# Kernel optimization log

Hardware: AMD Instinct MI355X
Metric: run time of the kernel (lower is better)

Reference implementation:

```python
import jax, jax.numpy as jnp
import numpy as np
from jax import lax

B, L, D_IN, H, D_OUT = 128, 1024, 64, 512, 64


def setup_inputs() -> dict:
    key = jax.random.key(0)
    ks = jax.random.split(key, 11)
    s_in = 1.0 / np.sqrt(D_IN)
    s_h = 1.0 / np.sqrt(H)
    return {
        "u": jax.random.normal(ks[0], (B, L, D_IN), jnp.float32),
        "W_in": jax.random.uniform(ks[1], (H, D_IN), jnp.float32, -s_in, s_in),
        "W_ih0": jax.random.uniform(ks[2], (H, H), jnp.float32, -s_h, s_h),
        "W_hh0": jax.random.uniform(ks[3], (H, H), jnp.float32, -s_h, s_h),
        "b_ih0": jax.random.uniform(ks[4], (H,), jnp.float32, -s_h, s_h),
        "b_hh0": jax.random.uniform(ks[5], (H,), jnp.float32, -s_h, s_h),
        "W_ih1": jax.random.uniform(ks[6], (H, H), jnp.float32, -s_h, s_h),
        "W_hh1": jax.random.uniform(ks[7], (H, H), jnp.float32, -s_h, s_h),
        "b_ih1": jax.random.uniform(ks[8], (H,), jnp.float32, -s_h, s_h),
        "b_hh1": jax.random.uniform(ks[9], (H,), jnp.float32, -s_h, s_h),
        "W_out": jax.random.uniform(ks[10], (D_OUT, H), jnp.float32, -s_h, s_h),
    }


def _rnn_layer(x, W_ih, W_hh, b):
    # x: [B, L, H]. Precompute input contribution as one big GEMM.
    xw = jnp.einsum("blh,gh->blg", x, W_ih) + b  # [B, L, H]
    xw_t = jnp.swapaxes(xw, 0, 1)  # [L, B, H] for scan over time

    def step(h, xt):
        h_new = jnp.tanh(xt + h @ W_hh.T)
        return h_new, h_new

    h0 = jnp.zeros((x.shape[0], W_hh.shape[0]), x.dtype)
    _, ys = lax.scan(step, h0, xw_t)
    return jnp.swapaxes(ys, 0, 1)  # [B, L, H]


def reference(u, W_in, W_ih0, W_hh0, b_ih0, b_hh0, W_ih1, W_hh1, b_ih1, b_hh1, W_out):
    x = jnp.einsum("bld,hd->blh", u, W_in)  # proj_in (no bias)
    x = _rnn_layer(x, W_ih0, W_hh0, b_ih0 + b_hh0)
    x = _rnn_layer(x, W_ih1, W_hh1, b_ih1 + b_hh1)
    y = jnp.einsum("blh,oh->blo", x, W_out)  # proj_out (no bias)
    return y
```

## Files before the change

### kernel.cpp

```cpp
#include <hip/hip_runtime.h>
#include <hip/hip_fp16.h>

#define B_   128
#define L_   1024
#define DIN  64
#define H_   512
#define DOUT 64

typedef _Float16 half8 __attribute__((ext_vector_type(8)));
typedef float    f32x4 __attribute__((ext_vector_type(4)));

#define FSTR 16
#define SPIN_CAP (1<<16)
#define POLL_CAP (1<<15)
#define POISON   0x7C00u

#define MFMA16(a,b,c) __builtin_amdgcn_mfma_f32_16x16x32_f16((a),(b),(c),0,0,0)
#define PINH8(x) asm volatile("" : "+v"(x))
#define AGENT_ST(p, v) __hip_atomic_store((p), (v), __ATOMIC_RELAXED, __HIP_MEMORY_SCOPE_AGENT)
#define AGENT_LD(p)    __hip_atomic_load((p), __ATOMIC_RELAXED, __HIP_MEMORY_SCOPE_AGENT)

__global__ void k_init(int* flags, unsigned int* hx0u, unsigned int* hx1u) {
    int i = blockIdx.x * blockDim.x + threadIdx.x;
    const int NR = 8 * 8 * 8192 / 2;
    if (i < NR) { hx0u[i] = 0x7C007C00u; hx1u[i] = 0x7C007C00u; }
    if (i < 104) flags[i * FSTR] = -1;
}

__global__ void k_prep_w(const float* __restrict__ whh0, const float* __restrict__ wih1,
                         const float* __restrict__ whh1, const float* __restrict__ wout,
                         const float* __restrict__ bih0, const float* __restrict__ bhh0,
                         const float* __restrict__ bih1, const float* __restrict__ bhh1,
                         _Float16* __restrict__ o0, _Float16* __restrict__ o1,
                         _Float16* __restrict__ o2, _Float16* __restrict__ o3,
                         float* __restrict__ b0s, float* __restrict__ b1s) {
    const int NW = H_ * H_;
    const int total = 3 * NW + DOUT * H_ + 2 * H_;
    int i  = blockIdx.x * blockDim.x + threadIdx.x;
    int st = gridDim.x * blockDim.x;
    for (; i < total; i += st) {
        if      (i < NW)            o0[i]          = (_Float16)whh0[i];
        else if (i < 2 * NW)        o1[i - NW]     = (_Float16)wih1[i - NW];
        else if (i < 3 * NW)        o2[i - 2 * NW] = (_Float16)whh1[i - 2 * NW];
        else if (i < 3 * NW + DOUT * H_) o3[i - 3 * NW] = (_Float16)wout[i - 3 * NW];
        else if (i < 3 * NW + DOUT * H_ + H_) {
            int j = i - (3 * NW + DOUT * H_);
            b0s[j] = bih0[j] + bhh0[j];
        } else {
            int j = i - (3 * NW + DOUT * H_ + H_);
            b1s[j] = bih1[j] + bhh1[j];
        }
    }
}

__global__ void k_wcomb(const float* __restrict__ wih0, const float* __restrict__ win,
                        _Float16* __restrict__ o) {
    int g = blockIdx.x;
    int d = threadIdx.x;
    float acc = 0.f;
    for (int h = 0; h < H_; ++h)
        acc += wih0[g * H_ + h] * win[h * DIN + d];
    o[g * DIN + d] = (_Float16)acc;
}

__device__ __forceinline__ int spin_geq(const int* fp, int tgt, int cached) {
    if (cached >= tgt) return cached;
    int v = AGENT_LD(fp);
    int it = 0;
    while (v < tgt && ++it < SPIN_CAP) v = AGENT_LD(fp);
    return v;
}

__device__ __forceinline__ float tanh_fast(float v) {
    float e = __expf(2.f * v);
    return 1.f - 2.f / (e + 1.f);
}

__device__ __forceinline__ void st16_sc(void* p, half8 v) {
    asm volatile("global_store_dwordx4 %0, %1, off sc0 sc1" :: "v"(p), "v"(v) : "memory");
}

__device__ __forceinline__ void ld4_sc(const _Float16* p0, const _Float16* p1,
                                       const _Float16* p2, const _Float16* p3,
                                       half8& a, half8& b, half8& c, half8& d) {
    asm volatile(
        "global_load_dwordx4 %0, %4, off sc0 sc1\n\t"
        "global_load_dwordx4 %1, %5, off sc0 sc1\n\t"
        "global_load_dwordx4 %2, %6, off sc0 sc1\n\t"
        "global_load_dwordx4 %3, %7, off sc0 sc1\n\t"
        "s_waitcnt vmcnt(0)"
        : "=&v"(a), "=&v"(b), "=&v"(c), "=&v"(d)
        : "v"(p0), "v"(p1), "v"(p2), "v"(p3) : "memory");
}
__device__ __forceinline__ void ld8_sc(const _Float16* p0, const _Float16* p1,
                                       const _Float16* p2, const _Float16* p3,
                                       const _Float16* p4, const _Float16* p5,
                                       const _Float16* p6, const _Float16* p7,
                                       half8& a, half8& b, half8& c, half8& d,
                                       half8& e, half8& f, half8& g, half8& h) {
    asm volatile(
        "global_load_dwordx4 %0, %8, off sc0 sc1\n\t"
        "global_load_dwordx4 %1, %9, off sc0 sc1\n\t"
        "global_load_dwordx4 %2, %10, off sc0 sc1\n\t"
        "global_load_dwordx4 %3, %11, off sc0 sc1\n\t"
        "global_load_dwordx4 %4, %12, off sc0 sc1\n\t"
        "global_load_dwordx4 %5, %13, off sc0 sc1\n\t"
        "global_load_dwordx4 %6, %14, off sc0 sc1\n\t"
        "global_load_dwordx4 %7, %15, off sc0 sc1\n\t"
        "s_waitcnt vmcnt(0)"
        : "=&v"(a), "=&v"(b), "=&v"(c), "=&v"(d),
          "=&v"(e), "=&v"(f), "=&v"(g), "=&v"(h)
        : "v"(p0), "v"(p1), "v"(p2), "v"(p3),
          "v"(p4), "v"(p5), "v"(p6), "v"(p7) : "memory");
}

__device__ __forceinline__ int chunk_ok(half8 h) {
    union { half8 v; unsigned short s[8]; } u; u.v = h;
    return u.s[0] != POISON;
}

__global__ __launch_bounds__(256, 1)
void k_pipeline(const float* __restrict__ u,
                const _Float16* __restrict__ wcomb,
                const _Float16* __restrict__ whh0w,
                const float* __restrict__ b0s,
                const _Float16* __restrict__ wih1w,
                const _Float16* __restrict__ whh1w,
                const float* __restrict__ b1s,
                const _Float16* __restrict__ woutw,
                float* __restrict__ out,
                _Float16* __restrict__ hx0,
                _Float16* __restrict__ hx1,
                int* __restrict__ flags) {
    const int bid = blockIdx.x;
    const int g = bid & 7, role = bid >> 3;
    const int tid = threadIdx.x;
    const int l = tid & 63, w = tid >> 6;
    const int l15 = l & 15, lg = l >> 4, kofs = lg * 8;
    const int b0 = g * 16;
    _Float16* hx0g = hx0 + (size_t)g * 65536;
    _Float16* hx1g = hx1 + (size_t)g * 65536;
    int* myctr = flags + bid * FSTR;

    __shared__ _Float16 pb0[16][520];
    __shared__ _Float16 pb1[16][520];
    __shared__ _Float16 hlt[16][136];

    union { unsigned short s[8]; half8 h; } pv;
#pragma unroll
    for (int i = 0; i < 8; ++i) pv.s[i] = POISON;
    const half8 poisonv = pv.h;

    const int rof0 = tid * 8;
    const int rof1 = rof0 + 2048;
    const int rof2 = rof0 + 4096;
    const int rof3 = rof0 + 6144;
    const int prw = tid >> 6;
    const int pcol = (tid & 63) * 8;

    if (role < 4) {
        const int s = role;
        const int col0 = s * 128 + w * 32;
        half8 whf[2][16], wcf[2][2];
#pragma unroll
        for (int nt = 0; nt < 2; ++nt) {
            const int n = col0 + nt * 16 + l15;
#pragma unroll
            for (int kt = 0; kt < 16; ++kt) {
                whf[nt][kt] = *(const half8*)(whh0w + (size_t)n * H_ + kt * 32 + kofs);
                PINH8(whf[nt][kt]);
            }
#pragma unroll
            for (int kt = 0; kt < 2; ++kt) {
                wcf[nt][kt] = *(const half8*)(wcomb + (size_t)n * DIN + kt * 32 + kofs);
                PINH8(wcf[nt][kt]);
            }
        }
        const float bv0 = b0s[col0 + l15], bv1 = b0s[col0 + 16 + l15];
        const int* gate = (tid < 12) ? flags + (g + 8 * tid) * FSTR : nullptr;
        int gcache = -1;
        const int oofs = (tid >> 4) * 512 + s * 128 + (tid & 15) * 8;

        for (int t = 0; t < L_; ++t) {
            if (t >= 4 && (t & 3) == 0 && gate) gcache = spin_geq(gate, t - 3, gcache);
            __syncthreads();
            st16_sc(hx0g + (size_t)((t + 2) & 7) * 8192 + oofs, poisonv);
            const float* up = u + ((size_t)(b0 + l15) * L_ + t) * DIN + kofs;
            f32x4 u0 = *(const f32x4*)(up);
            f32x4 u1 = *(const f32x4*)(up + 4);
            f32x4 u2 = *(const f32x4*)(up + 32);
            f32x4 u3 = *(const f32x4*)(up + 36);
            half8 ua0, ua1;
#pragma unroll
            for (int j = 0; j < 4; ++j) {
                ua0[j] = (_Float16)u0[j]; ua0[4 + j] = (_Float16)u1[j];
                ua1[j] = (_Float16)u2[j]; ua1[4 + j] = (_Float16)u3[j];
            }
            f32x4 acc0 = (f32x4){bv0, bv0, bv0, bv0};
            f32x4 acc1 = (f32x4){bv1, bv1, bv1, bv1};
            acc0 = MFMA16(ua0, wcf[0][0], acc0); acc0 = MFMA16(ua1, wcf[0][1], acc0);
            acc1 = MFMA16(ua0, wcf[1][0], acc1); acc1 = MFMA16(ua1, wcf[1][1], acc1);
            if (t > 0) {
                const _Float16* sb = hx0g + (size_t)((t - 1) & 7) * 8192;
                half8 c0, c1, c2, c3; int it = 0;
                for (;;) {
                    ld4_sc(sb + rof0, sb + rof1, sb + rof2, sb + rof3, c0, c1, c2, c3);
                    if ((chunk_ok(c0) & chunk_ok(c1) & chunk_ok(c2) & chunk_ok(c3))
                        || ++it > POLL_CAP) break;
                }
                *(half8*)&pb0[prw][pcol]      = c0;
                *(half8*)&pb0[prw + 4][pcol]  = c1;
                *(half8*)&pb0[prw + 8][pcol]  = c2;
                *(half8*)&pb0[prw + 12][pcol] = c3;
            }
            __syncthreads();
            if (tid == 0) AGENT_ST(myctr, t);
            if (t > 0) {
#pragma unroll
                for (int kt = 0; kt < 16; ++kt) {
                    half8 a = *(const half8*)&pb0[l15][kt * 32 + kofs];
                    acc0 = MFMA16(a, whf[0][kt], acc0);
                    acc1 = MFMA16(a, whf[1][kt], acc1);
                }
            }
            _Float16 th0[4], th1[4];
#pragma unroll
            for (int r = 0; r < 4; ++r) {
                th0[r] = (_Float16)tanh_fast(acc0[r]);
                th1[r] = (_Float16)tanh_fast(acc1[r]);
            }
#pragma unroll
            for (int r = 0; r < 4; ++r) {
                hlt[lg * 4 + r][w * 32 + l15]      = th0[r];
                hlt[lg * 4 + r][w * 32 + 16 + l15] = th1[r];
            }
            __syncthreads();
            half8 ch = *(const half8*)&hlt[tid >> 4][(tid & 15) * 8];
            asm volatile("s_waitcnt vmcnt(0)" ::: "memory");
            st16_sc(hx0g + (size_t)(t & 7) * 8192 + oofs, ch);
        }
    } else if (role < 12) {
        const int s = role - 4;
        const int n = s * 64 + w * 16 + l15;
        half8 wif[16], whf1[16];
#pragma unroll
        for (int kt = 0; kt < 16; ++kt) {
            wif[kt] = *(const half8*)(wih1w + (size_t)n * H_ + kt * 32 + kofs);
            PINH8(wif[kt]);
            whf1[kt] = *(const half8*)(whh1w + (size_t)n * H_ + kt * 32 + kofs);
            PINH8(whf1[kt]);
        }
        const float bv = b1s[n];
        const int* gate = (tid < 9) ? flags + (g + 8 * (4 + tid)) * FSTR : nullptr;
        int gcache = -1;
        const int oofs = (tid >> 3) * 512 + s * 64 + (tid & 7) * 8;

        for (int t = 0; t < L_; ++t) {
            if (t >= 4 && (t & 3) == 0 && gate) gcache = spin_geq(gate, t - 3, gcache);
            __syncthreads();
            if (tid < 128)
                st16_sc(hx1g + (size_t)((t + 2) & 7) * 8192 + oofs, poisonv);
            const _Float16* s0 = hx0g + (size_t)(t & 7) * 8192;
            if (t > 0) {
                const _Float16* s1 = hx1g + (size_t)((t - 1) & 7) * 8192;
                half8 d0, d1, d2, d3, e0, e1, e2, e3; int it = 0;
                for (;;) {
                    ld8_sc(s1 + rof0, s1 + rof1, s1 + rof2, s1 + rof3,
                           s0 + rof0, s0 + rof1, s0 + rof2, s0 + rof3,
                           d0, d1, d2, d3, e0, e1, e2, e3);
                    if ((chunk_ok(d0) & chunk_ok(d1) & chunk_ok(d2) & chunk_ok(d3)
                       & chunk_ok(e0) & chunk_ok(e1) & chunk_ok(e2) & chunk_ok(e3))
                        || ++it > POLL_CAP) break;
                }
                *(half8*)&pb1[prw][pcol]      = d0;
                *(half8*)&pb1[prw + 4][pcol]  = d1;
                *(half8*)&pb1[prw + 8][pcol]  = d2;
                *(half8*)&pb1[prw + 12][pcol] = d3;
                *(half8*)&pb0[prw][pcol]      = e0;
                *(half8*)&pb0[prw + 4][pcol]  = e1;
                *(half8*)&pb0[prw + 8][pcol]  = e2;
                *(half8*)&pb0[prw + 12][pcol] = e3;
            } else {
                half8 e0, e1, e2, e3; int it = 0;
                for (;;) {
                    ld4_sc(s0 + rof0, s0 + rof1, s0 + rof2, s0 + rof3, e0, e1, e2, e3);
                    if ((chunk_ok(e0) & chunk_ok(e1) & chunk_ok(e2) & chunk_ok(e3))
                        || ++it > POLL_CAP) break;
                }
                *(half8*)&pb0[prw][pcol]      = e0;
                *(half8*)&pb0[prw + 4][pcol]  = e1;
                *(half8*)&pb0[prw + 8][pcol]  = e2;
                *(half8*)&pb0[prw + 12][pcol] = e3;
            }
            __syncthreads();
            if (tid == 0) AGENT_ST(myctr, t);
            f32x4 acch = (f32x4){0.f, 0.f, 0.f, 0.f};
            f32x4 accx = (f32x4){bv, bv, bv, bv};
            if (t > 0) {
#pragma unroll
                for (int kt = 0; kt < 16; ++kt) {
                    half8 a1 = *(const half8*)&pb1[l15][kt * 32 + kofs];
                    acch = MFMA16(a1, whf1[kt], acch);
                    half8 a0 = *(const half8*)&pb0[l15][kt * 32 + kofs];
                    accx = MFMA16(a0, wif[kt], accx);
                }
            } else {
#pragma unroll
                for (int kt = 0; kt < 16; ++kt) {
                    half8 a0 = *(const half8*)&pb0[l15][kt * 32 + kofs];
                    accx = MFMA16(a0, wif[kt], accx);
                }
            }
            _Float16 th[4];
#pragma unroll
            for (int r = 0; r < 4; ++r) th[r] = (_Float16)tanh_fast(accx[r] + acch[r]);
#pragma unroll
            for (int r = 0; r < 4; ++r)
                hlt[lg * 4 + r][w * 16 + l15] = th[r];
            __syncthreads();
            if (tid < 128) {
                half8 ch = *(const half8*)&hlt[tid >> 3][(tid & 7) * 8];
                asm volatile("s_waitcnt vmcnt(0)" ::: "memory");
                st16_sc(hx1g + (size_t)(t & 7) * 8192 + oofs, ch);
            }
        }
    } else {
        const int n = w * 16 + l15;
        half8 wof[16];
#pragma unroll
        for (int kt = 0; kt < 16; ++kt) {
            wof[kt] = *(const half8*)(woutw + (size_t)n * H_ + kt * 32 + kofs);
            PINH8(wof[kt]);
        }
        for (int t = 0; t < L_; ++t) {
            __syncthreads();
            const _Float16* sb = hx1g + (size_t)(t & 7) * 8192;
            half8 c0, c1, c2, c3; int it = 0;
            for (;;) {
                ld4_sc(sb + rof0, sb + rof1, sb + rof2, sb + rof3, c0, c1, c2, c3);
                if ((chunk_ok(c0) & chunk_ok(c1) & chunk_ok(c2) & chunk_ok(c3))
                    || ++it > POLL_CAP) break;
            }
            *(half8*)&pb1[prw][pcol]      = c0;
            *(half8*)&pb1[prw + 4][pcol]  = c1;
            *(half8*)&pb1[prw + 8][pcol]  = c2;
            *(half8*)&pb1[prw + 12][pcol] = c3;
            __syncthreads();
            if (tid == 0) AGENT_ST(myctr, t);
            f32x4 acc = (f32x4){0.f, 0.f, 0.f, 0.f};
#pragma unroll
            for (int kt = 0; kt < 16; ++kt) {
                half8 a = *(const half8*)&pb1[l15][kt * 32 + kofs];
                acc = MFMA16(a, wof[kt], acc);
            }
#pragma unroll
            for (int r = 0; r < 4; ++r)
                out[((size_t)(b0 + lg * 4 + r) * L_ + t) * DOUT + n] = acc[r];
        }
    }
}

extern "C" void kernel_launch(void* const* d_in, const int* in_sizes, int n_in,
                              void* d_out, int out_size, void* d_ws, size_t ws_size,
                              hipStream_t stream) {
    const float* u    = (const float*)d_in[0];
    const float* Win  = (const float*)d_in[1];
    const float* Wih0 = (const float*)d_in[2];
    const float* Whh0 = (const float*)d_in[3];
    const float* bih0 = (const float*)d_in[4];
    const float* bhh0 = (const float*)d_in[5];
    const float* Wih1 = (const float*)d_in[6];
    const float* Whh1 = (const float*)d_in[7];
    const float* bih1 = (const float*)d_in[8];
    const float* bhh1 = (const float*)d_in[9];
    const float* Wout = (const float*)d_in[10];
    (void)in_sizes; (void)n_in; (void)out_size; (void)ws_size;

    char* ws = (char*)d_ws;
    size_t off = 0;
    auto alloc = [&](size_t bytes) {
        char* p = ws + off;
        off += (bytes + 255) & ~(size_t)255;
        return p;
    };
    _Float16* wcomb = (_Float16*)alloc((size_t)H_ * DIN * 2);
    _Float16* whh0h = (_Float16*)alloc((size_t)H_ * H_ * 2);
    _Float16* wih1h = (_Float16*)alloc((size_t)H_ * H_ * 2);
    _Float16* whh1h = (_Float16*)alloc((size_t)H_ * H_ * 2);
    _Float16* wouth = (_Float16*)alloc((size_t)DOUT * H_ * 2);
    float*    b0s   = (float*)alloc(H_ * 4);
    float*    b1s   = (float*)alloc(H_ * 4);
    _Float16* hx0   = (_Float16*)alloc((size_t)8 * 8 * 8192 * 2);
    _Float16* hx1   = (_Float16*)alloc((size_t)8 * 8 * 8192 * 2);
    int*      flags = (int*)alloc(104 * FSTR * 4);

    k_init<<<1024, 256, 0, stream>>>(flags, (unsigned int*)hx0, (unsigned int*)hx1);
    k_prep_w<<<1024, 256, 0, stream>>>(Whh0, Wih1, Whh1, Wout, bih0, bhh0, bih1, bhh1,
                                       whh0h, wih1h, whh1h, wouth, b0s, b1s);
    k_wcomb<<<512, 64, 0, stream>>>(Wih0, Win, wcomb);

    k_pipeline<<<104, 256, 0, stream>>>(u, wcomb, whh0h, b0s, wih1h, whh1h, b1s, wouth,
                                        (float*)d_out, hx0, hx1, flags);
}
```

Measured before the change: 2.380 ms.

## Merge per-step barriers, prefetch next u row, and pin weights inside loop

Removes the leading __syncthreads of each time step in all roles by moving the flow-control spin and the poison store after the poll/LDS-fill barrier. This cuts one barrier per step from the serial recurrence. Layer-0 blocks now load next step's input row one iteration ahead so the global load latency overlaps the current step. Register pinning of weights moves into the loop to keep them resident. hlt row padding changes from 136 to 140, which alters LDS bank mapping. Reordering the poison store and spin gate relative to the barrier risks new races in the ring-buffer protocol. It also shifts the trailing barrier in the output role to the end of the step.

Measured after the change: 2.441 ms. 1.03x slower.

```diff
diff --git a/kernel.cpp b/kernel.cpp
--- a/kernel.cpp
+++ b/kernel.cpp
@@ -144,7 +144,7 @@
 
     __shared__ _Float16 pb0[16][520];
     __shared__ _Float16 pb1[16][520];
-    __shared__ _Float16 hlt[16][136];
+    __shared__ _Float16 hlt[16][140];
 
     union { unsigned short s[8]; half8 h; } pv;
 #pragma unroll
@@ -166,35 +166,42 @@
         for (int nt = 0; nt < 2; ++nt) {
             const int n = col0 + nt * 16 + l15;
 #pragma unroll
-            for (int kt = 0; kt < 16; ++kt) {
+            for (int kt = 0; kt < 16; ++kt)
                 whf[nt][kt] = *(const half8*)(whh0w + (size_t)n * H_ + kt * 32 + kofs);
-                PINH8(whf[nt][kt]);
-            }
-#pragma unroll
-            for (int kt = 0; kt < 2; ++kt) {
+#pragma unroll
+            for (int kt = 0; kt < 2; ++kt)
                 wcf[nt][kt] = *(const half8*)(wcomb + (size_t)n * DIN + kt * 32 + kofs);
-                PINH8(wcf[nt][kt]);
-            }
         }
         const float bv0 = b0s[col0 + l15], bv1 = b0s[col0 + 16 + l15];
         const int* gate = (tid < 12) ? flags + (g + 8 * tid) * FSTR : nullptr;
         int gcache = -1;
         const int oofs = (tid >> 4) * 512 + s * 128 + (tid & 15) * 8;
 
+        const float* upbase = u + ((size_t)(b0 + l15) * L_) * DIN + kofs;
+        f32x4 un0 = *(const f32x4*)(upbase);
+        f32x4 un1 = *(const f32x4*)(upbase + 4);
+        f32x4 un2 = *(const f32x4*)(upbase + 32);
+        f32x4 un3 = *(const f32x4*)(upbase + 36);
+
         for (int t = 0; t < L_; ++t) {
-            if (t >= 4 && (t & 3) == 0 && gate) gcache = spin_geq(gate, t - 3, gcache);
-            __syncthreads();
-            st16_sc(hx0g + (size_t)((t + 2) & 7) * 8192 + oofs, poisonv);
-            const float* up = u + ((size_t)(b0 + l15) * L_ + t) * DIN + kofs;
-            f32x4 u0 = *(const f32x4*)(up);
-            f32x4 u1 = *(const f32x4*)(up + 4);
-            f32x4 u2 = *(const f32x4*)(up + 32);
-            f32x4 u3 = *(const f32x4*)(up + 36);
+#pragma unroll
+            for (int nt = 0; nt < 2; ++nt) {
+#pragma unroll
+                for (int kt = 0; kt < 16; ++kt) PINH8(whf[nt][kt]);
+                PINH8(wcf[nt][0]); PINH8(wcf[nt][1]);
+            }
             half8 ua0, ua1;
 #pragma unroll
             for (int j = 0; j < 4; ++j) {
-                ua0[j] = (_Float16)u0[j]; ua0[4 + j] = (_Float16)u1[j];
-                ua1[j] = (_Float16)u2[j]; ua1[4 + j] = (_Float16)u3[j];
+                ua0[j] = (_Float16)un0[j]; ua0[4 + j] = (_Float16)un1[j];
+                ua1[j] = (_Float16)un2[j]; ua1[4 + j] = (_Float16)un3[j];
+            }
+            if (t + 1 < L_) {
+                const float* up = upbase + (size_t)(t + 1) * DIN;
+                un0 = *(const f32x4*)(up);
+                un1 = *(const f32x4*)(up + 4);
+                un2 = *(const f32x4*)(up + 32);
+                un3 = *(const f32x4*)(up + 36);
             }
             f32x4 acc0 = (f32x4){bv0, bv0, bv0, bv0};
             f32x4 acc1 = (f32x4){bv1, bv1, bv1, bv1};
@@ -213,8 +220,10 @@
                 *(half8*)&pb0[prw + 8][pcol]  = c2;
                 *(half8*)&pb0[prw + 12][pcol] = c3;
             }
+            if (t >= 4 && (t & 3) == 0 && gate) gcache = spin_geq(gate, t - 3, gcache);
             __syncthreads();
             if (tid == 0) AGENT_ST(myctr, t);
+            st16_sc(hx0g + (size_t)((t + 2) & 7) * 8192 + oofs, poisonv);
             if (t > 0) {
 #pragma unroll
                 for (int kt = 0; kt < 16; ++kt) {
@@ -245,10 +254,8 @@
         half8 wif[16], whf1[16];
 #pragma unroll
         for (int kt = 0; kt < 16; ++kt) {
-            wif[kt] = *(const half8*)(wih1w + (size_t)n * H_ + kt * 32 + kofs);
-            PINH8(wif[kt]);
+            wif[kt]  = *(const half8*)(wih1w + (size_t)n * H_ + kt * 32 + kofs);
             whf1[kt] = *(const half8*)(whh1w + (size_t)n * H_ + kt * 32 + kofs);
-            PINH8(whf1[kt]);
         }
         const float bv = b1s[n];
         const int* gate = (tid < 9) ? flags + (g + 8 * (4 + tid)) * FSTR : nullptr;
@@ -256,10 +263,8 @@
         const int oofs = (tid >> 3) * 512 + s * 64 + (tid & 7) * 8;
 
         for (int t = 0; t < L_; ++t) {
-            if (t >= 4 && (t & 3) == 0 && gate) gcache = spin_geq(gate, t - 3, gcache);
-            __syncthreads();
-            if (tid < 128)
-                st16_sc(hx1g + (size_t)((t + 2) & 7) * 8192 + oofs, poisonv);
+#pragma unroll
+            for (int kt = 0; kt < 16; ++kt) { PINH8(wif[kt]); PINH8(whf1[kt]); }
             const _Float16* s0 = hx0g + (size_t)(t & 7) * 8192;
             if (t > 0) {
                 const _Float16* s1 = hx1g + (size_t)((t - 1) & 7) * 8192;
@@ -292,8 +297,11 @@
                 *(half8*)&pb0[prw + 8][pcol]  = e2;
                 *(half8*)&pb0[prw + 12][pcol] = e3;
             }
+            if (t >= 4 && (t & 3) == 0 && gate) gcache = spin_geq(gate, t - 3, gcache);
             __syncthreads();
             if (tid == 0) AGENT_ST(myctr, t);
+            if (tid < 128)
+                st16_sc(hx1g + (size_t)((t + 2) & 7) * 8192 + oofs, poisonv);
             f32x4 acch = (f32x4){0.f, 0.f, 0.f, 0.f};
             f32x4 accx = (f32x4){bv, bv, bv, bv};
             if (t > 0) {
@@ -328,12 +336,11 @@
         const int n = w * 16 + l15;
         half8 wof[16];
 #pragma unroll
-        for (int kt = 0; kt < 16; ++kt) {
+        for (int kt = 0; kt < 16; ++kt)
             wof[kt] = *(const half8*)(woutw + (size_t)n * H_ + kt * 32 + kofs);
-            PINH8(wof[kt]);
-        }
         for (int t = 0; t < L_; ++t) {
-            __syncthreads();
+#pragma unroll
+            for (int kt = 0; kt < 16; ++kt) PINH8(wof[kt]);
             const _Float16* sb = hx1g + (size_t)(t & 7) * 8192;
             half8 c0, c1, c2, c3; int it = 0;
             for (;;) {
@@ -356,6 +363,7 @@
 #pragma unroll
             for (int r = 0; r < 4; ++r)
                 out[((size_t)(b0 + lg * 4 + r) * L_ + t) * DOUT + n] = acc[r];
+            __syncthreads();
         }
     }
 }
```
